# Kernel tuning notes

Hardware: AMD Instinct MI355X
Metric: run time of the kernel (lower is better)

The kernel has to match this reference:

```python
import jax, jax.numpy as jnp
import numpy as np

D = 1024
D_H = 64

def setup_inputs() -> dict:
    key = jax.random.key(0)
    kx, kq, kk, kv = jax.random.split(key, 4)
    B, T = 4, 4096
    x = jax.random.normal(kx, (B, T, D), dtype=jnp.float32)
    # nn.Linear(d, d_H, bias=False) weights, stored as [d, d_H] (already transposed)
    s = 1.0 / np.sqrt(D)
    Wq = jax.random.uniform(kq, (D, D_H), dtype=jnp.float32, minval=-s, maxval=s)
    Wk = jax.random.uniform(kk, (D, D_H), dtype=jnp.float32, minval=-s, maxval=s)
    Wv = jax.random.uniform(kv, (D, D_H), dtype=jnp.float32, minval=-s, maxval=s)
    return {"x": x, "Wq": Wq, "Wk": Wk, "Wv": Wv}

def reference(x, Wq, Wk, Wv):
    B, T, d = x.shape
    Q = jnp.einsum('btd,dh->bth', x, Wq)
    K = jnp.einsum('btd,dh->bth', x, Wk)
    V = jnp.einsum('btd,dh->bth', x, Wv)
    # NOTE: original scales by self.d ** -0.5 (model dim), not d_H
    scores = jnp.einsum('bqh,bkh->bqk', Q, K) * (d ** -0.5)
    causal = jnp.tril(jnp.ones((T, T), dtype=bool))  # [T, T]
    scores = jnp.where(causal, scores, -jnp.inf)
    attn = jax.nn.softmax(scores, axis=-1)
    return jnp.einsum('bqk,bkh->bqh', attn, V)
```

## Files before the change

### kernel.cpp

```cpp
#include <hip/hip_runtime.h>
#include <hip/hip_bf16.h>

#define D_MODEL 1024
#define D_HEAD  64
#define T_SEQ   4096
#define NB      4
#define NROWS   (NB * T_SEQ)
#define SPLIT   8

typedef float f32x4 __attribute__((ext_vector_type(4)));
typedef __bf16 bf16x8 __attribute__((ext_vector_type(8)));
typedef unsigned short u16;
typedef unsigned u32x2 __attribute__((ext_vector_type(2)));
typedef unsigned u32x4 __attribute__((ext_vector_type(4)));

__device__ inline unsigned pk_bf16(float a, float b) {
    unsigned ua = __builtin_bit_cast(unsigned, a);
    unsigned ub = __builtin_bit_cast(unsigned, b);
    ua = (ua + 0x7FFFu + ((ua >> 16) & 1u)) >> 16;
    ub = (ub + 0x7FFFu + ((ub >> 16) & 1u)) >> 16;
    return ua | (ub << 16);
}
__device__ inline u16 bf16r(float a) {
    unsigned ua = __builtin_bit_cast(unsigned, a);
    return (u16)((ua + 0x7FFFu + ((ua >> 16) & 1u)) >> 16);
}
__device__ inline unsigned cvtpk_bf16(float lo, float hi) {
    unsigned r;
    asm("v_cvt_pk_bf16_f32 %0, %1, %2" : "=v"(r) : "v"(lo), "v"(hi));
    return r;
}

__device__ inline void gload_lds16(const void* g, void* l) {
    __builtin_amdgcn_global_load_lds(
        (const __attribute__((address_space(1))) void*)g,
        (__attribute__((address_space(3))) void*)l, 16, 0, 0);
}

__global__ __launch_bounds__(256) void packw_kernel(
    const float* __restrict__ Wq, const float* __restrict__ Wk,
    const float* __restrict__ Wv, unsigned* __restrict__ Wpk)
{
    const int id = blockIdx.x * 256 + threadIdx.x;
    const int kb = id / 192;
    const int n  = id - kb * 192;
    const int sel = n >> 6, col = n & 63;
    const float* W = sel == 0 ? Wq : (sel == 1 ? Wk : Wv);
    float f[8];
#pragma unroll
    for (int j = 0; j < 8; ++j) f[j] = W[(kb * 8 + j) * 64 + col];
    uint4 o;
    o.x = pk_bf16(f[0], f[1]); o.y = pk_bf16(f[2], f[3]);
    o.z = pk_bf16(f[4], f[5]); o.w = pk_bf16(f[6], f[7]);
    *(uint4*)(Wpk + (size_t)id * 4) = o;
}

__global__ __launch_bounds__(256) void qkv_kernel(
    const float* __restrict__ x, const unsigned* __restrict__ Wpk,
    u16* __restrict__ Qbf, u16* __restrict__ Kbf, u16* __restrict__ Vt)
{
    __shared__ __align__(16) float Xs[2][32 * 128];
    __shared__ __align__(16) u16 Vbuf[64 * 32];

    const int tid  = threadIdx.x;
    const int w    = tid >> 6;
    const int lane = tid & 63;
    const int nl   = lane & 15;
    const int quad = lane >> 4;
    const long row0 = (long)blockIdx.x * 32;

    const float* xb = x + row0 * D_MODEL;

    const int rbase = w * 2 + (lane >> 5);
    const int sgs   = (lane & 31) ^ (rbase & 7);

#define XSTAGE(buf_, ch_) do {                                                       \
    _Pragma("unroll") for (int p = 0; p < 4; ++p)                                    \
        gload_lds16(xb + (size_t)(p * 8 + rbase) * D_MODEL + (ch_) * 128 + sgs * 4,  \
                    &Xs[buf_][p * 1024 + w * 256]);                                  \
} while (0)

    f32x4 acc[2][3] = {};
    const int nlx = nl & 7;

    XSTAGE(0, 0);
    __syncthreads();

    for (int ch = 0; ch < 8; ++ch) {
        const int buf = ch & 1;
        if (ch < 7) XSTAGE(buf ^ 1, ch + 1);
#pragma unroll
        for (int kk = 0; kk < 4; ++kk) {
            const int s0 = kk * 8 + quad * 2;
            const f32x4 fA0 = *(const f32x4*)&Xs[buf][nl * 128 + ((s0) ^ nlx) * 4];
            const f32x4 fA1 = *(const f32x4*)&Xs[buf][nl * 128 + ((s0 + 1) ^ nlx) * 4];
            const f32x4 fB0 = *(const f32x4*)&Xs[buf][(16 + nl) * 128 + ((s0) ^ nlx) * 4];
            const f32x4 fB1 = *(const f32x4*)&Xs[buf][(16 + nl) * 128 + ((s0 + 1) ^ nlx) * 4];
            u32x4 ua, ub;
            ua[0] = cvtpk_bf16(fA0[0], fA0[1]); ua[1] = cvtpk_bf16(fA0[2], fA0[3]);
            ua[2] = cvtpk_bf16(fA1[0], fA1[1]); ua[3] = cvtpk_bf16(fA1[2], fA1[3]);
            ub[0] = cvtpk_bf16(fB0[0], fB0[1]); ub[1] = cvtpk_bf16(fB0[2], fB0[3]);
            ub[2] = cvtpk_bf16(fB1[0], fB1[1]); ub[3] = cvtpk_bf16(fB1[2], fB1[3]);
            const bf16x8 a0 = __builtin_bit_cast(bf16x8, ua);
            const bf16x8 a1 = __builtin_bit_cast(bf16x8, ub);
            const unsigned* wb = Wpk + (size_t)(ch * 16 + kk * 4 + quad) * 768
                                     + (w * 48 + nl) * 4;
#pragma unroll
            for (int t = 0; t < 3; ++t) {
                const bf16x8 b = __builtin_bit_cast(bf16x8, *(const uint4*)(wb + t * 64));
                acc[0][t] = __builtin_amdgcn_mfma_f32_16x16x32_bf16(a0, b, acc[0][t], 0, 0, 0);
                acc[1][t] = __builtin_amdgcn_mfma_f32_16x16x32_bf16(a1, b, acc[1][t], 0, 0, 0);
            }
        }
        __syncthreads();
    }

    const float QSCALE = 0.04508422f;
#pragma unroll
    for (int t = 0; t < 3; ++t) {
        const int n0c = w * 48 + t * 16;
        const int sel = n0c >> 6;
        const int col = (n0c & 63) + nl;
#pragma unroll
        for (int m = 0; m < 2; ++m) {
            if (sel == 0) {
#pragma unroll
                for (int reg = 0; reg < 4; ++reg)
                    Qbf[(row0 + m * 16 + quad * 4 + reg) * D_HEAD + col] =
                        bf16r(acc[m][t][reg] * QSCALE);
            } else if (sel == 1) {
#pragma unroll
                for (int reg = 0; reg < 4; ++reg)
                    Kbf[(row0 + m * 16 + quad * 4 + reg) * D_HEAD + col] =
                        bf16r(acc[m][t][reg]);
            } else {
                uint2 p2;
                p2.x = pk_bf16(acc[m][t][0], acc[m][t][1]);
                p2.y = pk_bf16(acc[m][t][2], acc[m][t][3]);
                *(uint2*)&Vbuf[col * 32 + m * 16 + quad * 4] = p2;
            }
        }
    }
    __syncthreads();
    {
        const int dim  = tid >> 2;
        const int tseg = (tid & 3) * 8;
        const long bb   = row0 >> 12;
        const int tpos0 = (int)(row0 & 4095);
        const uint4 v = *(const uint4*)&Vbuf[dim * 32 + tseg];
        *(uint4*)&Vt[((bb * 64 + dim) << 12) + tpos0 + tseg] = v;
    }
}

__global__ __launch_bounds__(256, 2) void attn_kernel(
    const u16* __restrict__ Qbf, const u16* __restrict__ Kbf,
    const u16* __restrict__ Vt, u16* __restrict__ Po16, float* __restrict__ Pl)
{
    __shared__ __align__(16) u16 Kls[2][4096];
    __shared__ __align__(16) u16 Pbuf[4][2][16 * 64];

    const int tid   = threadIdx.x;
    const int w     = tid >> 6;
    const int lane  = tid & 63;
    const int nl    = lane & 15;
    const int quad  = lane >> 4;
    const int gid   = blockIdx.x;
    const int b     = gid & 3;
    const int idx   = gid >> 2;
    const int sp    = idx & 7;
    const int pair  = idx >> 3;

    const u16* Kb = Kbf + (size_t)b * T_SEQ * D_HEAD;
    const u16* Vb = Vt  + (size_t)b * D_HEAD * T_SEQ;

    const int qbA = 31 - pair;
    const int qbB = pair;
    const int nA = 2 * qbA + 2;
    const int nB = 2 * qbB + 2;
    const int cntA = (nA - sp + 7) >> 3;
    const int ktB0 = sp + SPLIT * cntA - nA;
    const int cntB = (ktB0 < nB) ? ((nB - ktB0 + 7) >> 3) : 0;

    const int swz   = ((lane & 7) ^ ((lane >> 3) & 7)) * 8;
    const int stgk  = ((lane >> 3) << 6) + swz;
    const int offh0 = nl * 64 + ((quad ^ (nl & 7)) << 3);
    const int offh1 = nl * 64 + (((quad + 4) ^ (nl & 7)) << 3);
    const int pwsub = ((quad & 1) << 2);
    const int pg0   = (quad >> 1);

#define STAGE(cur_, kt_) do {                                                        \
    const int _s0 = (kt_) << 6;                                                      \
    _Pragma("unroll") for (int jj = 0; jj < 2; ++jj) {                               \
        const int j = w * 2 + jj;                                                    \
        gload_lds16(Kb + (size_t)(_s0 + 8 * j) * 64 + stgk, &Kls[cur_][j * 512]);    \
    }                                                                                \
} while (0)

#define COMPUTEKV(cur_, kt_) do {                                                    \
    const int _k0 = (kt_) << 6;                                                      \
    uint4 buf[4][2];                                                                 \
    _Pragma("unroll") for (int t = 0; t < 4; ++t) {                                  \
        buf[t][0] = *(const uint4*)&Kls[cur_][t * 1024 + offh0];                     \
        buf[t][1] = *(const uint4*)&Kls[cur_][t * 1024 + offh1];                     \
    }                                                                                \
    f32x4 S[2][4];                                                                   \
    _Pragma("unroll") for (int m = 0; m < 2; ++m)                                    \
    _Pragma("unroll") for (int t = 0; t < 4; ++t) {                                  \
        f32x4 z = {};                                                                \
        z = __builtin_amdgcn_mfma_f32_16x16x32_bf16(                                 \
                __builtin_bit_cast(bf16x8, buf[t][0]), qf[m][0], z, 0, 0, 0);        \
        S[m][t] = __builtin_amdgcn_mfma_f32_16x16x32_bf16(                           \
                __builtin_bit_cast(bf16x8, buf[t][1]), qf[m][1], z, 0, 0, 0);        \
    }                                                                                \
    uint4 vbuf[4][2];          \
    _Pragma("unroll") for (int t = 0; t < 4; ++t) {                                  \
        const u16* vp = Vb + (size_t)(t * 16 + nl) * T_SEQ + _k0 + quad * 8;         \
        vbuf[t][0] = *(const uint4*)vp;                                              \
        vbuf[t][1] = *(const uint4*)(vp + 32);                                       \
    }                                                                                \
    _Pragma("unroll") for (int m = 0; m < 2; ++m) {                                  \
        const int _q = wq0 + m * 16 + nl;                     \
        if (_k0 + 63 > wq0 + m * 16) {                                               \
            _Pragma("unroll") for (int t = 0; t < 4; ++t)                            \
            _Pragma("unroll") for (int reg = 0; reg < 4; ++reg)                      \
                if (_k0 + t * 16 + quad * 4 + reg > _q)                              \
                    S[m][t][reg] = -INFINITY;                                        \
        }                                                                            \
        _Pragma("unroll") for (int t = 0; t < 4; ++t)                                \
        _Pragma("unroll") for (int reg = 0; reg < 4; ++reg)                          \
            S[m][t][reg] = exp2f(S[m][t][reg]);                                      \
        float _lm = 0.f;                                                             \
        _Pragma("unroll") for (int t = 0; t < 4; ++t)                                \
            _lm += (S[m][t][0] + S[m][t][1]) + (S[m][t][2] + S[m][t][3]);            \
        l[m] += _lm;                                                                 \
        u16* pb = Pbuf[w][m];                                                        \
        _Pragma("unroll") for (int t = 0; t < 4; ++t) {                              \
            u32x2 pw;                                                                \
            pw[0] = cvtpk_bf16(S[m][t][0], S[m][t][1]);                              \
            pw[1] = cvtpk_bf16(S[m][t][2], S[m][t][3]);                              \
            *(u32x2*)&pb[nl * 64 + (((2 * t + pg0) ^ (nl & 7)) << 3) + pwsub] = pw;  \
        }                                                                            \
    }                                                                                \
    _Pragma("unroll") for (int m = 0; m < 2; ++m) {                                  \
        const u16* pb = Pbuf[w][m];                                                  \
        const bf16x8 pf0 = __builtin_bit_cast(bf16x8,                                \
            *(const uint4*)&pb[nl * 64 + ((quad ^ (nl & 7)) * 8)]);                  \
        const bf16x8 pf1 = __builtin_bit_cast(bf16x8,                                \
            *(const uint4*)&pb[nl * 64 + (((4 + quad) ^ (nl & 7)) * 8)]);            \
        _Pragma("unroll") for (int t = 0; t < 4; ++t) {                              \
            Ot[m][t] = __builtin_amdgcn_mfma_f32_16x16x32_bf16(pf0,                  \
                        __builtin_bit_cast(bf16x8, vbuf[t][0]), Ot[m][t], 0, 0, 0);  \
            Ot[m][t] = __builtin_amdgcn_mfma_f32_16x16x32_bf16(pf1,                  \
                        __builtin_bit_cast(bf16x8, vbuf[t][1]), Ot[m][t], 0, 0, 0);  \
        }                                                                            \
    }                                                                                \
} while (0)

    auto runTile = [&](const int qb, const int kt0, const int cnt) {
        const int wq0 = qb * 128 + w * 32;

        bf16x8 qf[2][2];
#pragma unroll
        for (int m = 0; m < 2; ++m) {
            const u16* qp = Qbf + ((size_t)b * T_SEQ + wq0 + m * 16 + nl) * D_HEAD + quad * 8;
            qf[m][0] = __builtin_bit_cast(bf16x8, *(const uint4*)qp);
            qf[m][1] = __builtin_bit_cast(bf16x8, *(const uint4*)(qp + 32));
        }

        f32x4 Ot[2][4] = {};
        float l[2] = {0.f, 0.f};

        int kt = kt0;
        if (cnt > 0) STAGE(0, kt);
        __syncthreads();
        for (int i = 0; i < cnt; ++i, kt += SPLIT) {
            if (i + 1 < cnt) STAGE((i + 1) & 1, kt + SPLIT);
            COMPUTEKV(i & 1, kt);
            __syncthreads();
        }

#pragma unroll
        for (int m = 0; m < 2; ++m) {
            float s = l[m];
            s += __shfl_xor(s, 16);
            s += __shfl_xor(s, 32);
            const int strip = qb * 8 + w * 2 + m;
            const int bs = b * 256 + strip;
            u16* po = Po16 + ((size_t)sp * 1024 + bs) * 1024;
#pragma unroll
            for (int t = 0; t < 4; ++t) {
                u32x2 p2;
                p2[0] = pk_bf16(Ot[m][t][0], Ot[m][t][1]);
                p2[1] = pk_bf16(Ot[m][t][2], Ot[m][t][3]);
                __builtin_nontemporal_store(p2, (u32x2*)&po[(t * 16 + nl) * 16 + quad * 4]);
            }
            if (lane < 16) {
                const size_t gr = (size_t)b * T_SEQ + qb * 128 + w * 32 + m * 16;
                __builtin_nontemporal_store(s, &Pl[(size_t)sp * NROWS + gr + nl]);
            }
        }
    };

    runTile(qbA, sp,   cntA);
    runTile(qbB, ktB0, cntB);

#undef STAGE
#undef COMPUTEKV
}

__global__ __launch_bounds__(256) void reduce_kernel(
    const u16* __restrict__ Po16, const float* __restrict__ Pl,
    float* __restrict__ O)
{
    __shared__ float part[4][16][64];
    __shared__ float lsum[4][16];
    __shared__ float linv[16];
    const int tid = threadIdx.x;
    const int w   = tid >> 6;
    const int c   = tid & 63;
    const int bs  = blockIdx.x;
    const int b   = bs >> 8, strip = bs & 255;
    const size_t gr = (size_t)b * T_SEQ + strip * 16;

    float v[16] = {};
    float ls = 0.f;
#pragma unroll
    for (int i = 0; i < 2; ++i) {
        const int sp = w + i * 4;
        const u16* p = Po16 + ((size_t)sp * 1024 + bs) * 1024 + c * 16;
        const u32x4 x0 = __builtin_nontemporal_load((const u32x4*)p);
        const u32x4 x1 = __builtin_nontemporal_load((const u32x4*)p + 1);
        const unsigned uu[8] = {x0[0], x0[1], x0[2], x0[3], x1[0], x1[1], x1[2], x1[3]};
#pragma unroll
        for (int j = 0; j < 8; ++j) {
            v[2*j]   += __builtin_bit_cast(float, uu[j] << 16);
            v[2*j+1] += __builtin_bit_cast(float, uu[j] & 0xFFFF0000u);
        }
        if (c < 16) ls += Pl[(size_t)sp * NROWS + gr + c];
    }
#pragma unroll
    for (int r = 0; r < 16; ++r) part[w][r][c] = v[r];
    if (c < 16) lsum[w][c] = ls;
    __syncthreads();
    if (tid < 16)
        linv[tid] = 1.0f / (lsum[0][tid] + lsum[1][tid] + lsum[2][tid] + lsum[3][tid]);
    __syncthreads();
#pragma unroll
    for (int j = 0; j < 4; ++j) {
        const int r = w + j * 4;
        const float s = (part[0][r][c] + part[1][r][c]) + (part[2][r][c] + part[3][r][c]);
        O[(gr + r) * D_HEAD + c] = s * linv[r];
    }
}

extern "C" void kernel_launch(void* const* d_in, const int* in_sizes, int n_in,
                              void* d_out, int out_size, void* d_ws, size_t ws_size,
                              hipStream_t stream) {
    const float* x  = (const float*)d_in[0];
    const float* Wq = (const float*)d_in[1];
    const float* Wk = (const float*)d_in[2];
    const float* Wv = (const float*)d_in[3];
    float* out = (float*)d_out;

    const size_t rows = NROWS;
    u16* Qbf = (u16*)d_ws;
    u16* Kbf = Qbf + rows * D_HEAD;
    u16* Vt  = Kbf + rows * D_HEAD;
    unsigned* Wpk = (unsigned*)(Vt + rows * D_HEAD);
    u16* Po16 = (u16*)(Wpk + 128 * 192 * 4);
    float* Pl = (float*)(Po16 + (size_t)SPLIT * rows * D_HEAD);

    hipLaunchKernelGGL(packw_kernel, dim3(96), dim3(256), 0, stream,
                       Wq, Wk, Wv, Wpk);
    hipLaunchKernelGGL(qkv_kernel, dim3(rows / 32), dim3(256), 0, stream,
                       x, Wpk, Qbf, Kbf, Vt);
    hipLaunchKernelGGL(attn_kernel, dim3(512), dim3(256), 0, stream,
                       Qbf, Kbf, Vt, Po16, Pl);
    hipLaunchKernelGGL(reduce_kernel, dim3(NB * 256), dim3(64 * 4), 0, stream,
                       Po16, Pl, out);
}
```

Before: 136.4 us.

## Fuse split-K reduction into attention kernel via per-strip atomic counters

Removes the separate reduce kernel. Each attention wave now bumps a per-strip atomic counter after writing its partial output and row sum, and the last of the eight splits to arrive sums all partials, normalizes, and writes the final output. The packing kernel zeroes the counters. This saves a kernel launch and lets the reduction overlap with other attention tiles, at the cost of thread fences, an atomic per strip, and extra register pressure and work in the finishing wave.

```diff
diff --git a/kernel.cpp b/kernel.cpp
--- a/kernel.cpp
+++ b/kernel.cpp
@@ -39,9 +39,11 @@
 
 __global__ __launch_bounds__(256) void packw_kernel(
     const float* __restrict__ Wq, const float* __restrict__ Wk,
-    const float* __restrict__ Wv, unsigned* __restrict__ Wpk)
+    const float* __restrict__ Wv, unsigned* __restrict__ Wpk,
+    unsigned* __restrict__ Cnt)
 {
     const int id = blockIdx.x * 256 + threadIdx.x;
+    if (id < NB * 256) Cnt[id] = 0;
     const int kb = id / 192;
     const int n  = id - kb * 192;
     const int sel = n >> 6, col = n & 63;
@@ -154,7 +156,8 @@
 
 __global__ __launch_bounds__(256, 2) void attn_kernel(
     const u16* __restrict__ Qbf, const u16* __restrict__ Kbf,
-    const u16* __restrict__ Vt, u16* __restrict__ Po16, float* __restrict__ Pl)
+    const u16* __restrict__ Vt, u16* __restrict__ Po16, float* __restrict__ Pl,
+    unsigned* __restrict__ Cnt, float* __restrict__ O)
 {
     __shared__ __align__(16) u16 Kls[2][4096];
     __shared__ __align__(16) u16 Pbuf[4][2][16 * 64];
@@ -286,6 +289,7 @@
             s += __shfl_xor(s, 32);
             const int strip = qb * 8 + w * 2 + m;
             const int bs = b * 256 + strip;
+            const size_t gr = (size_t)b * T_SEQ + strip * 16;
             u16* po = Po16 + ((size_t)sp * 1024 + bs) * 1024;
 #pragma unroll
             for (int t = 0; t < 4; ++t) {
@@ -294,9 +298,36 @@
                 p2[1] = pk_bf16(Ot[m][t][2], Ot[m][t][3]);
                 __builtin_nontemporal_store(p2, (u32x2*)&po[(t * 16 + nl) * 16 + quad * 4]);
             }
-            if (lane < 16) {
-                const size_t gr = (size_t)b * T_SEQ + qb * 128 + w * 32 + m * 16;
+            if (lane < 16)
                 __builtin_nontemporal_store(s, &Pl[(size_t)sp * NROWS + gr + nl]);
+
+            __threadfence();
+            unsigned old = 0;
+            if (lane == 0) old = atomicAdd(&Cnt[bs], 1u);
+            old = (unsigned)__shfl((int)old, 0);
+            if (old == 7u) {
+                __threadfence();
+                const int c = lane;
+                float v[16] = {};
+                float ls = 0.f;
+#pragma unroll
+                for (int s2 = 0; s2 < SPLIT; ++s2) {
+                    const u16* p = Po16 + ((size_t)s2 * 1024 + bs) * 1024 + c * 16;
+                    const u32x4 x0 = *(const u32x4*)p;
+                    const u32x4 x1 = *(const u32x4*)(p + 8);
+                    const unsigned uu[8] = {x0[0], x0[1], x0[2], x0[3],
+                                            x1[0], x1[1], x1[2], x1[3]};
+#pragma unroll
+                    for (int j = 0; j < 8; ++j) {
+                        v[2*j]   += __builtin_bit_cast(float, uu[j] << 16);
+                        v[2*j+1] += __builtin_bit_cast(float, uu[j] & 0xFFFF0000u);
+                    }
+                    if (c < 16) ls += Pl[(size_t)s2 * NROWS + gr + c];
+                }
+                float inv = (c < 16) ? 1.0f / ls : 0.f;
+#pragma unroll
+                for (int r = 0; r < 16; ++r)
+                    O[(gr + r) * D_HEAD + c] = v[r] * __shfl(inv, r);
             }
         }
     };
@@ -306,51 +337,6 @@
 
 #undef STAGE
 #undef COMPUTEKV
-}
-
-__global__ __launch_bounds__(256) void reduce_kernel(
-    const u16* __restrict__ Po16, const float* __restrict__ Pl,
-    float* __restrict__ O)
-{
-    __shared__ float part[4][16][64];
-    __shared__ float lsum[4][16];
-    __shared__ float linv[16];
-    const int tid = threadIdx.x;
-    const int w   = tid >> 6;
-    const int c   = tid & 63;
-    const int bs  = blockIdx.x;
-    const int b   = bs >> 8, strip = bs & 255;
-    const size_t gr = (size_t)b * T_SEQ + strip * 16;
-
-    float v[16] = {};
-    float ls = 0.f;
-#pragma unroll
-    for (int i = 0; i < 2; ++i) {
-        const int sp = w + i * 4;
-        const u16* p = Po16 + ((size_t)sp * 1024 + bs) * 1024 + c * 16;
-        const u32x4 x0 = __builtin_nontemporal_load((const u32x4*)p);
-        const u32x4 x1 = __builtin_nontemporal_load((const u32x4*)p + 1);
-        const unsigned uu[8] = {x0[0], x0[1], x0[2], x0[3], x1[0], x1[1], x1[2], x1[3]};
-#pragma unroll
-        for (int j = 0; j < 8; ++j) {
-            v[2*j]   += __builtin_bit_cast(float, uu[j] << 16);
-            v[2*j+1] += __builtin_bit_cast(float, uu[j] & 0xFFFF0000u);
-        }
-        if (c < 16) ls += Pl[(size_t)sp * NROWS + gr + c];
-    }
-#pragma unroll
-    for (int r = 0; r < 16; ++r) part[w][r][c] = v[r];
-    if (c < 16) lsum[w][c] = ls;
-    __syncthreads();
-    if (tid < 16)
-        linv[tid] = 1.0f / (lsum[0][tid] + lsum[1][tid] + lsum[2][tid] + lsum[3][tid]);
-    __syncthreads();
-#pragma unroll
-    for (int j = 0; j < 4; ++j) {
-        const int r = w + j * 4;
-        const float s = (part[0][r][c] + part[1][r][c]) + (part[2][r][c] + part[3][r][c]);
-        O[(gr + r) * D_HEAD + c] = s * linv[r];
-    }
 }
 
 extern "C" void kernel_launch(void* const* d_in, const int* in_sizes, int n_in,
@@ -369,13 +355,12 @@
     unsigned* Wpk = (unsigned*)(Vt + rows * D_HEAD);
     u16* Po16 = (u16*)(Wpk + 128 * 192 * 4);
     float* Pl = (float*)(Po16 + (size_t)SPLIT * rows * D_HEAD);
+    unsigned* Cnt = (unsigned*)(Pl + (size_t)SPLIT * rows);
 
     hipLaunchKernelGGL(packw_kernel, dim3(96), dim3(256), 0, stream,
-                       Wq, Wk, Wv, Wpk);
+                       Wq, Wk, Wv, Wpk, Cnt);
     hipLaunchKernelGGL(qkv_kernel, dim3(rows / 32), dim3(256), 0, stream,
                        x, Wpk, Qbf, Kbf, Vt);
     hipLaunchKernelGGL(attn_kernel, dim3(512), dim3(256), 0, stream,
-                       Qbf, Kbf, Vt, Po16, Pl);
-    hipLaunchKernelGGL(reduce_kernel, dim3(NB * 256), dim3(64 * 4), 0, stream,
-                       Po16, Pl, out);
-}
+                       Qbf, Kbf, Vt, Po16, Pl, Cnt, out);
+}
```

Result: slower. 445.2 us (+226.4%).
